# Kernel tuning notes

Measured on AMD Instinct MI355X. Metric: run time of the kernel, lower is better.

Reference implementation:

```python
import jax, jax.numpy as jnp
import numpy as np

NUM_NEURONS = 256
NUM_SAMPLES = 512
MAX_SPIKES = 32
N_STEPS = 32          # fixed RK4 steps per spike round (stands in for adaptive Tsit5)
ALPHA = 0.03
V_RESET = 1.0
T0 = 0.0


def setup_inputs() -> dict:
    key = jax.random.key(0)
    ks = jax.random.split(key, 7)
    input_current = jax.random.normal(ks[0], (NUM_NEURONS,), dtype=jnp.float32)
    # _build_w with network=all-False: uniform(minval=0.5), mask sets nothing
    w = jax.random.uniform(ks[1], (NUM_NEURONS, NUM_NEURONS), minval=0.5, maxval=1.0, dtype=jnp.float32)
    mu = jax.random.uniform(ks[2], (2,), minval=0.5, maxval=1.0, dtype=jnp.float32)
    v0 = jax.random.normal(ks[3], (NUM_NEURONS,), dtype=jnp.float32)
    i0 = jax.random.normal(ks[4], (NUM_NEURONS,), dtype=jnp.float32)
    # s0 = log(U) - alpha  (always < 0)
    s0 = (jnp.log(jax.random.uniform(ks[5], (NUM_SAMPLES, NUM_NEURONS), minval=1e-6, maxval=1.0)) - ALPHA).astype(jnp.float32)
    # pre-drawn stochastic resets, one per (spike round, sample, neuron)
    reset_s = (jnp.log(jax.random.uniform(ks[6], (MAX_SPIKES, NUM_SAMPLES, NUM_NEURONS), minval=1e-6, maxval=1.0)) - ALPHA).astype(jnp.float32)
    return dict(input_current=input_current, w=w, mu=mu, v0=v0, i0=i0, s0=s0, reset_s=reset_s, t1=2)


def _drift(y, ic, mu1, mu2):
    # y: [samples, neurons, 3] = (v, i, s)
    v, i = y[..., 0], y[..., 1]
    dv = mu1 * (i + ic - v)
    di = -mu2 * i
    ds = jax.nn.sigmoid(v)  # intensity_fn(v)
    return jnp.stack([dv, di, ds], axis=-1)


def reference(input_current, w, mu, v0, i0, s0, reset_s, t1):
    t1f = jnp.float32(t1)
    mu1, mu2 = mu[0], mu[1]
    ic = input_current  # constant-in-time input current, [neurons]

    y0 = jnp.concatenate([
        jnp.broadcast_to(v0, (NUM_SAMPLES, NUM_NEURONS))[..., None],
        jnp.broadcast_to(i0, (NUM_SAMPLES, NUM_NEURONS))[..., None],
        s0[..., None]], axis=-1)  # [samples, neurons, 3]

    def rk4(y, h):
        k1 = _drift(y, ic, mu1, mu2)
        k2 = _drift(y + 0.5 * h * k1, ic, mu1, mu2)
        k3 = _drift(y + 0.5 * h * k2, ic, mu1, mu2)
        k4 = _drift(y + h * k3, ic, mu1, mu2)
        return y + (h / 6.0) * (k1 + 2.0 * k2 + 2.0 * k3 + k4)

    def round_body(carry, reset_k):
        t0s, y_in = carry                      # t0s: [samples]
        dt = (t1f - t0s) / N_STEPS             # per-sample step size
        h = dt[:, None, None]

        def step(sc, _):
            t, y, done, tev, yev, emask = sc
            y_new = rk4(y, h)
            y_new = jnp.where(done[:, None, None], y, y_new)  # freeze after event
            s_prev, s_new = y[..., 2], y_new[..., 2]
            crossed = s_new > 0.0                              # cond_fn root: s crosses 0
            trig = crossed.any(axis=1) & (~done)
            idx = jnp.argmax(s_new, axis=1)                    # event neuron (first/largest crossing)
            sp = jnp.take_along_axis(s_prev, idx[:, None], 1)[:, 0]
            sn = jnp.take_along_axis(s_new, idx[:, None], 1)[:, 0]
            frac = jnp.clip(sp / (sp - sn + 1e-12), 0.0, 1.0)  # linear root estimate (Newton stand-in)
            t_c = t + frac * dt
            y_c = y + frac[:, None, None] * (y_new - y)
            tev = jnp.where(trig, t_c, tev)
            yev = jnp.where(trig[:, None, None], y_c, yev)
            emask = jnp.where(trig[:, None], crossed, emask)
            y = jnp.where(trig[:, None, None], y_c, y_new)
            done = done | trig
            return (t + dt, y, done, tev, yev, emask), None

        done0 = jnp.zeros((NUM_SAMPLES,), bool)
        tev0 = jnp.full((NUM_SAMPLES,), jnp.inf, jnp.float32)
        em0 = jnp.zeros((NUM_SAMPLES, NUM_NEURONS), bool)
        (_, yend, done, tev, yev, emask), _ = jax.lax.scan(
            step, (t0s, y_in, done0, tev0, y_in, em0), None, length=N_STEPS)

        tev = jnp.where(done, tev, t1f)                 # no event -> sol.ts[-1] = t1
        yev = jnp.where(done[:, None, None], yev, yend)

        # trans_fn: spike reset + synaptic jump w[event_idx]
        eidx = jnp.argmax(emask, axis=1)
        w_row = jnp.where(done[:, None], w[eidx], 0.0)  # zero if no event happened
        v_t = yev[..., 0] - jnp.where(emask, V_RESET, 0.0)
        i_t = yev[..., 1] + w_row
        s_t = jnp.minimum(jnp.where(emask, reset_k, yev[..., 2]), 0.0)
        y_next = jnp.stack([v_t, i_t, s_t], axis=-1)
        return (tev, y_next), (tev, yev, emask)

    t0s = jnp.full((NUM_SAMPLES,), T0, jnp.float32)
    _, (tevs, yevs, emasks) = jax.lax.scan(jax.checkpoint(round_body), (t0s, y0), reset_s)

    spike_times = jnp.transpose(tevs, (1, 0))            # [samples, max_spikes]
    spike_values = jnp.transpose(yevs, (1, 0, 2, 3))     # [samples, max_spikes, neurons, 3]
    spike_marks = jnp.transpose(emasks, (1, 0, 2))       # [samples, max_spikes, neurons]
    return spike_times, spike_values, spike_marks
```

## Files before the change

kernel.cpp:

```cpp
#include <hip/hip_runtime.h>
#include <math.h>

#define NN 256
#define NS 512
#define MS 32
#define NSTEP 32
#define VRESET 1.0f

__device__ __forceinline__ float sigf(float x) {
    float e = __expf(-x);
    return __builtin_amdgcn_rcpf(1.0f + e);
}

__device__ __forceinline__ void block_sync_lds() {
    asm volatile("s_waitcnt lgkmcnt(0)" ::: "memory");
    __builtin_amdgcn_s_barrier();
    asm volatile("" ::: "memory");
}

__device__ __forceinline__ void rk4step(float v, float ii, float s,
                                        float ic, float mu1, float mu2,
                                        float dt, float hh, float h6,
                                        float& vn, float& in_, float& sn)
{
    float kv1 = mu1 * (ii + ic - v);
    float ki1 = -mu2 * ii;
    float ks1 = sigf(v);
    float v2 = v + hh * kv1;
    float i2 = ii + hh * ki1;
    float kv2 = mu1 * (i2 + ic - v2);
    float ki2 = -mu2 * i2;
    float ks2 = sigf(v2);
    float v3 = v + hh * kv2;
    float i3 = ii + hh * ki2;
    float kv3 = mu1 * (i3 + ic - v3);
    float ki3 = -mu2 * i3;
    float ks3 = sigf(v3);
    float v4 = v + dt * kv3;
    float i4 = ii + dt * ki3;
    float kv4 = mu1 * (i4 + ic - v4);
    float ki4 = -mu2 * i4;
    float ks4 = sigf(v4);
    vn  = v  + h6 * (kv1 + 2.0f * kv2 + 2.0f * kv3 + kv4);
    in_ = ii + h6 * (ki1 + 2.0f * ki2 + 2.0f * ki3 + ki4);
    sn  = s  + h6 * (ks1 + 2.0f * ks2 + 2.0f * ks3 + ks4);
}

__global__ __launch_bounds__(256) void snn_kernel(
    const float* __restrict__ ic_g,
    const float* __restrict__ w,
    const float* __restrict__ mu,
    const float* __restrict__ v0,
    const float* __restrict__ i0,
    const float* __restrict__ s0,
    const float* __restrict__ reset_s,
    const int*   __restrict__ t1p,
    float* __restrict__ out)
{
    const int tid  = threadIdx.x;
    const int lane = tid & 63;
    const int wid  = tid >> 6;
    const int samp = blockIdx.x;
    const float mu1 = mu[0];
    const float mu2 = mu[1];
    const float t1f = (float)t1p[0];

    __shared__ int4 s_flag[4];
    __shared__ __align__(16) float s_sn[2][NN];
    __shared__ __align__(16) float s_sp[2][NN];

    float v  = v0[tid];
    float ii = i0[tid];
    float s  = s0[samp * NN + tid];
    const float ic = ic_g[tid];
    float t0 = 0.0f;

    float* times = out;
    float* vals  = out + (size_t)NS * MS;
    float* marks = out + (size_t)NS * MS * (1 + NN * 3);

    for (int r = 0; r < MS; ++r) {
        const int buf = r & 1;
        const float rs = reset_s[((size_t)r * NS + samp) * NN + tid];

        const float dt = (t1f - t0) / (float)NSTEP;
        float tev = t1f;
        float yv = v, yi = ii, ys = s;
        bool  em = false;
        bool  done = false;
        float wr = 0.0f;

        if (dt != 0.0f) {
            const float hh = 0.5f * dt;
            const float h6 = dt * (1.0f / 6.0f);

            float pv = v, pi_ = ii, ps = s;
            float cv, ci, cs;
            rk4step(pv, pi_, ps, ic, mu1, mu2, dt, hh, h6, cv, ci, cs);
            float t = t0;

            for (int st = 0; st < NSTEP; ++st) {
                s_sn[buf][tid] = cs;
                s_sp[buf][tid] = ps;
                unsigned long long bl = __ballot(cs > 0.0f);
                if (lane == 0) {
                    int meta = (bl != 0ull)
                        ? ((((wid << 6) + (int)__builtin_ctzll(bl)) << 1) | 1)
                        : 0;
                    ((int*)&s_flag[st & 3])[wid] = meta;
                }

                float kv1 = mu1 * (ci + ic - cv);
                float ki1 = -mu2 * ci;
                float ks1 = sigf(cv);
                float v2 = cv + hh * kv1;
                float i2 = ci + hh * ki1;
                float kv2 = mu1 * (i2 + ic - v2);
                float ki2 = -mu2 * i2;
                float ks2 = sigf(v2);

                __builtin_amdgcn_sched_barrier(0);
                block_sync_lds();
                __builtin_amdgcn_sched_barrier(0);

                int4 f = s_flag[st & 3];

                float v3 = cv + hh * kv2;
                float i3 = ci + hh * ki2;
                float kv3 = mu1 * (i3 + ic - v3);
                float ki3 = -mu2 * i3;
                float ks3 = sigf(v3);
                float v4 = cv + dt * kv3;
                float i4 = ci + dt * ki3;
                float kv4 = mu1 * (i4 + ic - v4);
                float ki4 = -mu2 * i4;
                float ks4 = sigf(v4);
                float nv  = cv + h6 * (kv1 + 2.0f * kv2 + 2.0f * kv3 + kv4);
                float ni  = ci + h6 * (ki1 + 2.0f * ki2 + 2.0f * ki3 + ki4);
                float ns_ = cs + h6 * (ks1 + 2.0f * ks2 + 2.0f * ks3 + ks4);

                if ((f.x | f.y | f.z | f.w) & 1) {
                    const float4 q =
                        *(const float4*)&s_sn[buf][lane << 2];
                    int e0 = (f.x & 1) ? (f.x >> 1) : (2 * NN);
                    int e1 = (f.y & 1) ? (f.y >> 1) : (2 * NN);
                    int e2 = (f.z & 1) ? (f.z >> 1) : (2 * NN);
                    int e3 = (f.w & 1) ? (f.w >> 1) : (2 * NN);
                    int ea = e0 < e1 ? e0 : e1;
                    int eb = e2 < e3 ? e2 : e3;
                    int eidx = ea < eb ? ea : eb;
                    wr = w[eidx * NN + tid];

                    unsigned bx = __float_as_uint(q.x);
                    unsigned by = __float_as_uint(q.y);
                    unsigned bz = __float_as_uint(q.z);
                    unsigned bw = __float_as_uint(q.w);
                    unsigned k0 = (bx & 0x80000000u) ? ~bx : (bx | 0x80000000u);
                    unsigned k1 = (by & 0x80000000u) ? ~by : (by | 0x80000000u);
                    unsigned k2 = (bz & 0x80000000u) ? ~bz : (bz | 0x80000000u);
                    unsigned k3 = (bw & 0x80000000u) ? ~bw : (bw | 0x80000000u);
                    unsigned km = k0; int pos = 0;
                    if (k1 > km) { km = k1; pos = 1; }
                    if (k2 > km) { km = k2; pos = 2; }
                    if (k3 > km) { km = k3; pos = 3; }
                    unsigned red = km;
#pragma unroll
                    for (int off = 32; off >= 1; off >>= 1) {
                        unsigned o = __shfl_xor(red, off);
                        red = (o > red) ? o : red;
                    }
                    unsigned long long cm = __ballot(km == red);
                    int L = (int)__builtin_ctzll(cm);
                    int wpos = __builtin_amdgcn_readlane(pos, L);
                    int bn = (L << 2) + wpos;

                    float bv  = s_sn[buf][bn];
                    float bsp = s_sp[buf][bn];
                    float frac = bsp / (bsp - bv + 1e-12f);
                    frac = fminf(fmaxf(frac, 0.0f), 1.0f);
                    tev = t + frac * dt;
                    yv = pv  + frac * (cv - pv);
                    yi = pi_ + frac * (ci - pi_);
                    ys = ps  + frac * (cs - ps);
                    em = (cs > 0.0f);
                    done = true;
                    break;
                }

                if (st + 1 < NSTEP) {
                    pv = cv; pi_ = ci; ps = cs;
                    cv = nv; ci = ni; cs = ns_;
                    t += dt;
                }
            }

            if (!done) { yv = cv; yi = ci; ys = cs; }
        }

        const int sr = samp * MS + r;
        if (tid == 0) times[sr] = tev;
        {
            float* p = vals + ((size_t)sr * NN + tid) * 3;
            p[0] = yv;
            p[1] = yi;
            p[2] = ys;
            marks[(size_t)sr * NN + tid] = em ? 1.0f : 0.0f;
        }

        if (done) {
            v  = yv - (em ? VRESET : 0.0f);
            ii = yi + wr;
            float sres = em ? rs : ys;
            s = fminf(sres, 0.0f);
        } else {
            v = yv; ii = yi;
            s = fminf(ys, 0.0f);
        }
        t0 = tev;
    }
}

extern "C" void kernel_launch(void* const* d_in, const int* in_sizes, int n_in,
                              void* d_out, int out_size, void* d_ws, size_t ws_size,
                              hipStream_t stream) {
    const float* ic      = (const float*)d_in[0];
    const float* w       = (const float*)d_in[1];
    const float* mu      = (const float*)d_in[2];
    const float* v0      = (const float*)d_in[3];
    const float* i0      = (const float*)d_in[4];
    const float* s0      = (const float*)d_in[5];
    const float* reset_s = (const float*)d_in[6];
    const int*   t1p     = (const int*)d_in[7];
    float* out = (float*)d_out;

    snn_kernel<<<dim3(NS), dim3(256), 0, stream>>>(ic, w, mu, v0, i0, s0,
                                                   reset_s, t1p, out);
}
```

Before: 132.9 us.

## Replace per-step block barrier with tagged LDS mailbox flags and spin-wait

Removes the workgroup s_barrier from each RK4 step. Each wave now publishes a tagged event flag into a per-step mailbox slot and computes the next step before polling for the other waves' flags, with double-buffered LDS state per round and per step parity. The aim is to let waves run ahead and hide synchronisation latency behind computation. In exchange the code depends on volatile spin-waits with s_sleep and on LDS memory-ordering assumptions, and it does extra speculative work.

```diff
diff --git a/kernel.cpp b/kernel.cpp
--- a/kernel.cpp
+++ b/kernel.cpp
@@ -6,16 +6,11 @@
 #define MS 32
 #define NSTEP 32
 #define VRESET 1.0f
+#define TAGSH 10
 
 __device__ __forceinline__ float sigf(float x) {
     float e = __expf(-x);
     return __builtin_amdgcn_rcpf(1.0f + e);
-}
-
-__device__ __forceinline__ void block_sync_lds() {
-    asm volatile("s_waitcnt lgkmcnt(0)" ::: "memory");
-    __builtin_amdgcn_s_barrier();
-    asm volatile("" ::: "memory");
 }
 
 __device__ __forceinline__ void rk4step(float v, float ii, float s,
@@ -65,9 +60,15 @@
     const float mu2 = mu[1];
     const float t1f = (float)t1p[0];
 
-    __shared__ int4 s_flag[4];
-    __shared__ __align__(16) float s_sn[2][NN];
-    __shared__ __align__(16) float s_sp[2][NN];
+    __shared__ int4  s_mb[2][NSTEP + 1];
+    __shared__ __align__(16) float s_sn[2][2][NN];
+    __shared__ __align__(16) float s_sp[2][2][NN];
+
+    {
+        int* mf = (int*)s_mb;
+        for (int i = tid; i < 2 * (NSTEP + 1) * 4; i += 256) mf[i] = 0;
+    }
+    __syncthreads();
 
     float v  = v0[tid];
     float ii = i0[tid];
@@ -80,7 +81,8 @@
     float* marks = out + (size_t)NS * MS * (1 + NN * 3);
 
     for (int r = 0; r < MS; ++r) {
-        const int buf = r & 1;
+        const int rp = r & 1;
+        const int rtag = r * (NSTEP + 1);
         const float rs = reset_s[((size_t)r * NS + samp) * NN + tid];
 
         const float dt = (t1f - t0) / (float)NSTEP;
@@ -99,53 +101,62 @@
             rk4step(pv, pi_, ps, ic, mu1, mu2, dt, hh, h6, cv, ci, cs);
             float t = t0;
 
-            for (int st = 0; st < NSTEP; ++st) {
-                s_sn[buf][tid] = cs;
-                s_sp[buf][tid] = ps;
+            {
+                s_sn[rp][1][tid] = cs;
+                s_sp[rp][1][tid] = s;
                 unsigned long long bl = __ballot(cs > 0.0f);
+                asm volatile("s_waitcnt lgkmcnt(0)" ::: "memory");
                 if (lane == 0) {
                     int meta = (bl != 0ull)
                         ? ((((wid << 6) + (int)__builtin_ctzll(bl)) << 1) | 1)
                         : 0;
-                    ((int*)&s_flag[st & 3])[wid] = meta;
-                }
-
-                float kv1 = mu1 * (ci + ic - cv);
-                float ki1 = -mu2 * ci;
-                float ks1 = sigf(cv);
-                float v2 = cv + hh * kv1;
-                float i2 = ci + hh * ki1;
-                float kv2 = mu1 * (i2 + ic - v2);
-                float ki2 = -mu2 * i2;
-                float ks2 = sigf(v2);
-
+                    ((volatile int*)&s_mb[rp][1])[wid] =
+                        ((rtag + 1) << TAGSH) | meta;
+                }
+            }
+
+            for (int st = 1; st <= NSTEP; ++st) {
+                int4 f = s_mb[rp][st];
+
+                const bool morestep = (st < NSTEP);
+                float nv = 0.0f, ni = 0.0f, ns_ = 0.0f;
+                if (morestep) {
+                    rk4step(cv, ci, cs, ic, mu1, mu2, dt, hh, h6,
+                            nv, ni, ns_);
+                    s_sn[rp][(st + 1) & 1][tid] = ns_;
+                    s_sp[rp][(st + 1) & 1][tid] = cs;
+                    unsigned long long bl = __ballot(ns_ > 0.0f);
+                    asm volatile("s_waitcnt lgkmcnt(0)" ::: "memory");
+                    if (lane == 0) {
+                        int meta = (bl != 0ull)
+                            ? ((((wid << 6) + (int)__builtin_ctzll(bl)) << 1) | 1)
+                            : 0;
+                        ((volatile int*)&s_mb[rp][st + 1])[wid] =
+                            ((rtag + st + 1) << TAGSH) | meta;
+                    }
+                }
+
+                const int want = rtag + st;
+                if ((f.x >> TAGSH) != want || (f.y >> TAGSH) != want ||
+                    (f.z >> TAGSH) != want || (f.w >> TAGSH) != want) {
+                    volatile int* mp = (volatile int*)&s_mb[rp][st];
+                    do {
+                        __builtin_amdgcn_s_sleep(1);
+                        f.x = mp[0]; f.y = mp[1]; f.z = mp[2]; f.w = mp[3];
+                    } while ((f.x >> TAGSH) != want || (f.y >> TAGSH) != want ||
+                             (f.z >> TAGSH) != want || (f.w >> TAGSH) != want);
+                }
                 __builtin_amdgcn_sched_barrier(0);
-                block_sync_lds();
-                __builtin_amdgcn_sched_barrier(0);
-
-                int4 f = s_flag[st & 3];
-
-                float v3 = cv + hh * kv2;
-                float i3 = ci + hh * ki2;
-                float kv3 = mu1 * (i3 + ic - v3);
-                float ki3 = -mu2 * i3;
-                float ks3 = sigf(v3);
-                float v4 = cv + dt * kv3;
-                float i4 = ci + dt * ki3;
-                float kv4 = mu1 * (i4 + ic - v4);
-                float ki4 = -mu2 * i4;
-                float ks4 = sigf(v4);
-                float nv  = cv + h6 * (kv1 + 2.0f * kv2 + 2.0f * kv3 + kv4);
-                float ni  = ci + h6 * (ki1 + 2.0f * ki2 + 2.0f * ki3 + ki4);
-                float ns_ = cs + h6 * (ks1 + 2.0f * ks2 + 2.0f * ks3 + ks4);
+                asm volatile("" ::: "memory");
 
                 if ((f.x | f.y | f.z | f.w) & 1) {
+                    const int sp2 = st & 1;
                     const float4 q =
-                        *(const float4*)&s_sn[buf][lane << 2];
-                    int e0 = (f.x & 1) ? (f.x >> 1) : (2 * NN);
-                    int e1 = (f.y & 1) ? (f.y >> 1) : (2 * NN);
-                    int e2 = (f.z & 1) ? (f.z >> 1) : (2 * NN);
-                    int e3 = (f.w & 1) ? (f.w >> 1) : (2 * NN);
+                        *(const float4*)&s_sn[rp][sp2][lane << 2];
+                    int e0 = (f.x & 1) ? ((f.x >> 1) & 0xFF) : (2 * NN);
+                    int e1 = (f.y & 1) ? ((f.y >> 1) & 0xFF) : (2 * NN);
+                    int e2 = (f.z & 1) ? ((f.z >> 1) & 0xFF) : (2 * NN);
+                    int e3 = (f.w & 1) ? ((f.w >> 1) & 0xFF) : (2 * NN);
                     int ea = e0 < e1 ? e0 : e1;
                     int eb = e2 < e3 ? e2 : e3;
                     int eidx = ea < eb ? ea : eb;
@@ -174,8 +185,8 @@
                     int wpos = __builtin_amdgcn_readlane(pos, L);
                     int bn = (L << 2) + wpos;
 
-                    float bv  = s_sn[buf][bn];
-                    float bsp = s_sp[buf][bn];
+                    float bv  = s_sn[rp][sp2][bn];
+                    float bsp = s_sp[rp][sp2][bn];
                     float frac = bsp / (bsp - bv + 1e-12f);
                     frac = fminf(fmaxf(frac, 0.0f), 1.0f);
                     tev = t + frac * dt;
@@ -187,7 +198,7 @@
                     break;
                 }
 
-                if (st + 1 < NSTEP) {
+                if (morestep) {
                     pv = cv; pi_ = ci; ps = cs;
                     cv = nv; ci = ni; cs = ns_;
                     t += dt;
```

Result: slower. 156.6 us (+17.8%).
